# Performance work log

Measured on AMD Instinct MI355X. Metric: run time of the kernel, lower is better.

The kernel has to match this reference:

```python
import jax, jax.numpy as jnp
import numpy as np

BATCH, IN_F, OUT_F, K = 16384, 1024, 1024, 256


def setup_inputs() -> dict:
    key = jax.random.key(0)
    kx, kw, kp = jax.random.split(key, 3)
    x = jax.random.normal(kx, (BATCH, IN_F), dtype=jnp.float32)
    weights = jax.random.normal(kw, (OUT_F, IN_F), dtype=jnp.float32)
    P = jax.random.normal(kp, (K, IN_F), dtype=jnp.float32)  # LSH projection matrix (K, in_features)
    return {"x": x, "weights": weights, "P": P}


def _codes(unit, P):
    # SimHash binary codes in {-1, +1}: sign of random projections
    return jnp.where(unit @ P.T >= 0, 1.0, -1.0).astype(unit.dtype)


def reference(x, weights, P):
    eps = jnp.finfo(x.dtype).eps
    # normalize rows of x and weights
    x_norms = jnp.linalg.norm(x, axis=-1, keepdims=True) + eps        # (B, 1)
    x_unit = x / x_norms
    w_norms = jnp.linalg.norm(weights, axis=-1, keepdims=True) + eps  # (M, 1)
    w_unit = weights / w_norms
    # hash codes
    codes_x = _codes(x_unit, P)   # (B, K)
    codes_w = _codes(w_unit, P)   # (M, K)
    # agreement-based cosine estimate: dot/K = 1 - 2*hamming_frac
    dot = codes_x @ codes_w.T                                   # (B, M)
    k = jnp.asarray(P.shape[0], dtype=x.dtype)
    half_pi = jnp.asarray(np.pi * 0.5, dtype=x.dtype)
    cos_est = jnp.cos(half_pi * (1.0 - dot / k))                # (B, M)
    return x_norms * w_norms.T * cos_est                        # (B, M)
```

## Files before the change

kernel.cpp:

```cpp
#include <hip/hip_runtime.h>
#include <hip/hip_bf16.h>
#include <math.h>

#define BATCH 16384
#define OUTF  1024
#define INF   1024
#define KPROJ 256
#define MTOT  (BATCH + OUTF)

#define GBM 32
#define GBN 128
#define GBK 64
#define NKT (INF / GBK)

#define NZ_THRESH 0.15f

typedef unsigned int       u32;
typedef unsigned long long u64;
typedef unsigned short     u16;
typedef _Float16           f16;
typedef __attribute__((ext_vector_type(8))) _Float16 f16x8;
typedef __attribute__((ext_vector_type(4))) float    f32x4;

#define SCHED0() __builtin_amdgcn_sched_barrier(0)

__device__ __forceinline__ void gl_lds16(const void* g, void* l) {
    __builtin_amdgcn_global_load_lds(
        (const __attribute__((address_space(1))) u32*)g,
        (__attribute__((address_space(3))) u32*)l, 16, 0, 0);
}

__global__ __launch_bounds__(256) void prep_p(const float* __restrict__ P,
                                              f16* __restrict__ Bp) {
    const int wave = threadIdx.x >> 6, lane = threadIdx.x & 63;
    const int pr = blockIdx.x * 4 + wave;
    const float4* v = (const float4*)(P + (size_t)pr * INF);
    ushort4* d = (ushort4*)(Bp + (size_t)pr * INF);
#pragma unroll
    for (int q = 0; q < 4; ++q) {
        float4 f = v[lane + 64 * q];
        ushort4 o;
        o.x = __builtin_bit_cast(u16, (f16)f.x);
        o.y = __builtin_bit_cast(u16, (f16)f.y);
        o.z = __builtin_bit_cast(u16, (f16)f.z);
        o.w = __builtin_bit_cast(u16, (f16)f.w);
        d[lane + 64 * q] = o;
    }
}

__global__ __launch_bounds__(256, 4) void gemm_signs(const float* __restrict__ X,
                                                     const float* __restrict__ W,
                                                     const f16* __restrict__ Bp,
                                                     const float* __restrict__ Pf,
                                                     u64* __restrict__ cx,
                                                     u64* __restrict__ cw,
                                                     float* __restrict__ xn,
                                                     float* __restrict__ wn) {
    __shared__ __align__(16) unsigned char ldsA[GBM * 8 * 16];
    __shared__ __align__(16) unsigned char ldsB[GBN * 8 * 16];
    __shared__ u16 sw[GBM][8];
    __shared__ float nsq[GBM][8];

    const int t    = threadIdx.x;
    const int wid  = t >> 6, lane = t & 63;
    const int l4   = lane >> 4, l15 = lane & 15;
    const int wc   = wid;
    const int sb   = (blockIdx.x & 7) * ((MTOT / GBM) * 2 / 8) + (blockIdx.x >> 3);
    const int bm   = sb >> 1;
    const int bn0  = (sb & 1) * GBN;
    const int am0  = bm * GBM;

    const int ra = t >> 3, sa = t & 7, ca = sa ^ (ra & 7);
    const float* Asrc = (am0 < BATCH) ? X + (size_t)am0 * INF
                                      : W + (size_t)(am0 - BATCH) * INF;
    const float* aRow = Asrc + (size_t)ra * INF + ca * 8;

    const f16* bsrc[4];
#pragma unroll
    for (int i = 0; i < 4; ++i) {
        const int g = (i * 4 + wid) * 64 + lane;
        const int row = g >> 3, sl = g & 7, cb = sl ^ (row & 7);
        bsrc[i] = Bp + (size_t)(bn0 + row) * INF + cb * 8;
    }

    f32x4 acc[2][2] = {};
    float ssq = 0.0f;
    float4 pf0 = *(const float4*)(aRow);
    float4 pf1 = *(const float4*)(aRow + 4);

    for (int kt = 0; kt < NKT; ++kt) {
        ssq += pf0.x * pf0.x + pf0.y * pf0.y + pf0.z * pf0.z + pf0.w * pf0.w +
               pf1.x * pf1.x + pf1.y * pf1.y + pf1.z * pf1.z + pf1.w * pf1.w;
        {
            f16x8 h;
            h[0] = (f16)pf0.x; h[1] = (f16)pf0.y; h[2] = (f16)pf0.z; h[3] = (f16)pf0.w;
            h[4] = (f16)pf1.x; h[5] = (f16)pf1.y; h[6] = (f16)pf1.z; h[7] = (f16)pf1.w;
            *(f16x8*)(ldsA + t * 16) = h;
        }
#pragma unroll
        for (int i = 0; i < 4; ++i)
            gl_lds16(bsrc[i] + kt * GBK, ldsB + (i * 4 + wid) * 1024);
        SCHED0();
        if (kt + 1 < NKT) {
            pf0 = *(const float4*)(aRow + (kt + 1) * GBK);
            pf1 = *(const float4*)(aRow + (kt + 1) * GBK + 4);
            SCHED0();
            asm volatile("s_waitcnt vmcnt(2) lgkmcnt(0)" ::: "memory");
        } else {
            asm volatile("s_waitcnt vmcnt(0) lgkmcnt(0)" ::: "memory");
        }
        SCHED0();
        __builtin_amdgcn_s_barrier();
        SCHED0();
#pragma unroll
        for (int ks = 0; ks < 2; ++ks) {
            f16x8 af[2], bf[2];
#pragma unroll
            for (int i = 0; i < 2; ++i) {
                const int row = i * 16 + l15;
                const int slot = (ks * 4 + l4) ^ (row & 7);
                af[i] = *(const f16x8*)(ldsA + row * 128 + slot * 16);
            }
#pragma unroll
            for (int j = 0; j < 2; ++j) {
                const int col = wc * 32 + j * 16 + l15;
                const int slot = (ks * 4 + l4) ^ (col & 7);
                bf[j] = *(const f16x8*)(ldsB + col * 128 + slot * 16);
            }
#pragma unroll
            for (int i = 0; i < 2; ++i)
#pragma unroll
                for (int j = 0; j < 2; ++j)
                    acc[i][j] = __builtin_amdgcn_mfma_f32_16x16x32_f16(af[i], bf[j], acc[i][j], 0, 0, 0);
        }
        SCHED0();
        __builtin_amdgcn_s_barrier();
        SCHED0();
    }

    nsq[ra][sa] = ssq;

#pragma unroll
    for (int i = 0; i < 2; ++i)
#pragma unroll
        for (int j = 0; j < 2; ++j)
#pragma unroll
            for (int q = 0; q < 4; ++q) {
                const float v = acc[i][j][q];
                int bit = (v >= 0.0f) ? 1 : 0;
                u64 fl = __ballot(fabsf(v) < NZ_THRESH);
                while (fl) {
                    const int src = __ffsll((long long)fl) - 1;
                    fl &= fl - 1;
                    const int lrow = i * 16 + ((src >> 4) << 2) + q;
                    const int col  = bn0 + wc * 32 + j * 16 + (src & 15);
                    const float* xr = Asrc + (size_t)lrow * INF + lane * 16;
                    const float* pr = Pf + (size_t)col * INF + lane * 16;
                    double s = 0.0;
#pragma unroll
                    for (int c4 = 0; c4 < 4; ++c4) {
                        float4 xa = *(const float4*)(xr + c4 * 4);
                        float4 pa = *(const float4*)(pr + c4 * 4);
                        s += (double)xa.x * pa.x + (double)xa.y * pa.y +
                             (double)xa.z * pa.z + (double)xa.w * pa.w;
                    }
#pragma unroll
                    for (int off = 32; off; off >>= 1) s += __shfl_xor(s, off, 64);
                    if (lane == src) bit = (s >= 0.0) ? 1 : 0;
                }
                const u64 b = __ballot(bit != 0);
                if (l15 == 0)
                    sw[i * 16 + l4 * 4 + q][wc * 2 + j] = (u16)(b >> (l4 * 16));
            }
    if (bn0 == 0 && t < GBM) {
        const float* p = nsq[t];
        float s = ((p[0] + p[1]) + (p[2] + p[3])) + ((p[4] + p[5]) + (p[6] + p[7]));
        const float n = sqrtf(s) + 1.1920929e-07f;
        const int grow = am0 + t;
        if (grow < BATCH) xn[grow] = n; else wn[grow - BATCH] = n;
    }
    __syncthreads();
    if (t < 64) {
        const int r = t >> 1, wsel = t & 1;
        const u64 val = *(const u64*)&sw[r][wsel * 4];
        const int grow = am0 + r;
        const int word = (sb & 1) * 2 + wsel;
        if (grow < BATCH) cx[(size_t)grow * 4 + word] = val;
        else              cw[(size_t)(grow - BATCH) * 4 + word] = val;
    }
}

__global__ __launch_bounds__(256) void popc_out(const u64* __restrict__ cx,
                                                const u64* __restrict__ cw,
                                                const float* __restrict__ xn,
                                                const float* __restrict__ wn,
                                                float* __restrict__ out) {
    __shared__ float lut[257];
    __shared__ u64 cxs[64][4];
    __shared__ float xns[64];
    const int t = threadIdx.x;

    lut[t] = (float)cos((double)t * (3.14159265358979323846 / 256.0));
    if (t == 0) lut[256] = -1.0f;

    const int r0 = blockIdx.x * 64;
    cxs[t >> 2][t & 3] = cx[(size_t)r0 * 4 + t];
    if (t < 64) xns[t] = xn[r0 + t];

    const ulonglong4* cwv4 = (const ulonglong4*)cw;
    ulonglong4 c0 = cwv4[4 * t + 0];
    ulonglong4 c1 = cwv4[4 * t + 1];
    ulonglong4 c2 = cwv4[4 * t + 2];
    ulonglong4 c3 = cwv4[4 * t + 3];
    float4 wnr = ((const float4*)wn)[t];

    __syncthreads();

    float4* outv = (float4*)out;
    const size_t obase = (size_t)r0 * (OUTF / 4) + t;
#pragma unroll 4
    for (int r = 0; r < 64; ++r) {
        const u64 a0 = cxs[r][0], a1 = cxs[r][1], a2 = cxs[r][2], a3 = cxs[r][3];
        const float sx = xns[r];
        float4 o;
        o.x = sx * wnr.x * lut[__popcll(a0 ^ c0.x) + __popcll(a1 ^ c0.y) +
                               __popcll(a2 ^ c0.z) + __popcll(a3 ^ c0.w)];
        o.y = sx * wnr.y * lut[__popcll(a0 ^ c1.x) + __popcll(a1 ^ c1.y) +
                               __popcll(a2 ^ c1.z) + __popcll(a3 ^ c1.w)];
        o.z = sx * wnr.z * lut[__popcll(a0 ^ c2.x) + __popcll(a1 ^ c2.y) +
                               __popcll(a2 ^ c2.z) + __popcll(a3 ^ c2.w)];
        o.w = sx * wnr.w * lut[__popcll(a0 ^ c3.x) + __popcll(a1 ^ c3.y) +
                               __popcll(a2 ^ c3.z) + __popcll(a3 ^ c3.w)];
        outv[obase + (size_t)r * (OUTF / 4)] = o;
    }
}

extern "C" void kernel_launch(void* const* d_in, const int* in_sizes, int n_in,
                              void* d_out, int out_size, void* d_ws, size_t ws_size,
                              hipStream_t stream) {
    const float* x = (const float*)d_in[0];
    const float* w = (const float*)d_in[1];
    const float* P = (const float*)d_in[2];
    float* out = (float*)d_out;

    char* ws = (char*)d_ws;
    f16*  Bp = (f16*)ws;
    u64*  cx = (u64*)(ws + 524288);
    u64*  cw = (u64*)(ws + 1048576);
    float* xn = (float*)(ws + 1081344);
    float* wn = (float*)(ws + 1146880);

    prep_p<<<KPROJ / 4, 256, 0, stream>>>(P, Bp);

    gemm_signs<<<(MTOT / GBM) * 2, 256, 0, stream>>>(x, w, Bp, P, cx, cw, xn, wn);

    popc_out<<<BATCH / 64, 256, 0, stream>>>(cx, cw, xn, wn, out);
}
```

Baseline: 61.85 us.

## Double-buffer B tiles and batch A prefetch four k-steps ahead in sign GEMM

Reworks the sign-GEMM main loop into a fully unrolled schedule. The B tile in LDS is now double-buffered, so the next slice's global-to-LDS copy is issued before the current slice's MFMAs run. A-operand fp32 loads are fetched in groups of four k-steps into two alternating register sets. The aim is to hide global load latency behind compute. The cost is more registers and LDS, so the occupancy hint drops from 4 to 3 waves per SIMD, and many steps still wait on vmcnt(0), which may limit the overlap.

```diff
diff --git a/kernel.cpp b/kernel.cpp
--- a/kernel.cpp
+++ b/kernel.cpp
@@ -12,6 +12,7 @@
 #define GBN 128
 #define GBK 64
 #define NKT (INF / GBK)
+#define NWG ((MTOT / GBM) * 2)
 
 #define NZ_THRESH 0.15f
 
@@ -48,7 +49,7 @@
     }
 }
 
-__global__ __launch_bounds__(256, 4) void gemm_signs(const float* __restrict__ X,
+__global__ __launch_bounds__(256, 3) void gemm_signs(const float* __restrict__ X,
                                                      const float* __restrict__ W,
                                                      const f16* __restrict__ Bp,
                                                      const float* __restrict__ Pf,
@@ -57,7 +58,7 @@
                                                      float* __restrict__ xn,
                                                      float* __restrict__ wn) {
     __shared__ __align__(16) unsigned char ldsA[GBM * 8 * 16];
-    __shared__ __align__(16) unsigned char ldsB[GBN * 8 * 16];
+    __shared__ __align__(16) unsigned char ldsB[2 * GBN * 8 * 16];
     __shared__ u16 sw[GBM][8];
     __shared__ float nsq[GBM][8];
 
@@ -65,7 +66,7 @@
     const int wid  = t >> 6, lane = t & 63;
     const int l4   = lane >> 4, l15 = lane & 15;
     const int wc   = wid;
-    const int sb   = (blockIdx.x & 7) * ((MTOT / GBM) * 2 / 8) + (blockIdx.x >> 3);
+    const int sb   = (blockIdx.x & 7) * (NWG / 8) + (blockIdx.x >> 3);
     const int bm   = sb >> 1;
     const int bn0  = (sb & 1) * GBN;
     const int am0  = bm * GBM;
@@ -85,58 +86,107 @@
 
     f32x4 acc[2][2] = {};
     float ssq = 0.0f;
-    float4 pf0 = *(const float4*)(aRow);
-    float4 pf1 = *(const float4*)(aRow + 4);
-
-    for (int kt = 0; kt < NKT; ++kt) {
-        ssq += pf0.x * pf0.x + pf0.y * pf0.y + pf0.z * pf0.z + pf0.w * pf0.w +
-               pf1.x * pf1.x + pf1.y * pf1.y + pf1.z * pf1.z + pf1.w * pf1.w;
-        {
-            f16x8 h;
-            h[0] = (f16)pf0.x; h[1] = (f16)pf0.y; h[2] = (f16)pf0.z; h[3] = (f16)pf0.w;
-            h[4] = (f16)pf1.x; h[5] = (f16)pf1.y; h[6] = (f16)pf1.z; h[7] = (f16)pf1.w;
-            *(f16x8*)(ldsA + t * 16) = h;
-        }
-#pragma unroll
-        for (int i = 0; i < 4; ++i)
-            gl_lds16(bsrc[i] + kt * GBK, ldsB + (i * 4 + wid) * 1024);
-        SCHED0();
-        if (kt + 1 < NKT) {
-            pf0 = *(const float4*)(aRow + (kt + 1) * GBK);
-            pf1 = *(const float4*)(aRow + (kt + 1) * GBK + 4);
-            SCHED0();
-            asm volatile("s_waitcnt vmcnt(2) lgkmcnt(0)" ::: "memory");
-        } else {
-            asm volatile("s_waitcnt vmcnt(0) lgkmcnt(0)" ::: "memory");
-        }
-        SCHED0();
-        __builtin_amdgcn_s_barrier();
-        SCHED0();
-#pragma unroll
-        for (int ks = 0; ks < 2; ++ks) {
-            f16x8 af[2], bf[2];
-#pragma unroll
-            for (int i = 0; i < 2; ++i) {
-                const int row = i * 16 + l15;
-                const int slot = (ks * 4 + l4) ^ (row & 7);
-                af[i] = *(const f16x8*)(ldsA + row * 128 + slot * 16);
-            }
-#pragma unroll
-            for (int j = 0; j < 2; ++j) {
-                const int col = wc * 32 + j * 16 + l15;
-                const int slot = (ks * 4 + l4) ^ (col & 7);
-                bf[j] = *(const f16x8*)(ldsB + col * 128 + slot * 16);
-            }
-#pragma unroll
-            for (int i = 0; i < 2; ++i)
-#pragma unroll
-                for (int j = 0; j < 2; ++j)
-                    acc[i][j] = __builtin_amdgcn_mfma_f32_16x16x32_f16(af[i], bf[j], acc[i][j], 0, 0, 0);
-        }
-        SCHED0();
-        __builtin_amdgcn_s_barrier();
-        SCHED0();
-    }
+    float4 qa0, qa1, qa2, qa3, qa4, qa5, qa6, qa7;
+    float4 qb0, qb1, qb2, qb3, qb4, qb5, qb6, qb7;
+
+#define ALOAD_G(P, G)                                                         \
+    P##0 = *(const float4*)(aRow + ((G) * 4 + 0) * 64);                       \
+    P##1 = *(const float4*)(aRow + ((G) * 4 + 0) * 64 + 4);                   \
+    P##2 = *(const float4*)(aRow + ((G) * 4 + 1) * 64);                       \
+    P##3 = *(const float4*)(aRow + ((G) * 4 + 1) * 64 + 4);                   \
+    P##4 = *(const float4*)(aRow + ((G) * 4 + 2) * 64);                       \
+    P##5 = *(const float4*)(aRow + ((G) * 4 + 2) * 64 + 4);                   \
+    P##6 = *(const float4*)(aRow + ((G) * 4 + 3) * 64);                       \
+    P##7 = *(const float4*)(aRow + ((G) * 4 + 3) * 64 + 4);
+
+#define ASTAGE(Q0, Q1)                                                        \
+    {                                                                         \
+        ssq += Q0.x * Q0.x + Q0.y * Q0.y + Q0.z * Q0.z + Q0.w * Q0.w +        \
+               Q1.x * Q1.x + Q1.y * Q1.y + Q1.z * Q1.z + Q1.w * Q1.w;         \
+        f16x8 h;                                                              \
+        h[0] = (f16)Q0.x; h[1] = (f16)Q0.y; h[2] = (f16)Q0.z; h[3] = (f16)Q0.w;\
+        h[4] = (f16)Q1.x; h[5] = (f16)Q1.y; h[6] = (f16)Q1.z; h[7] = (f16)Q1.w;\
+        *(f16x8*)(ldsA + t * 16) = h;                                         \
+    }
+
+#define BISSUE(S1)                                                            \
+    {                                                                         \
+        _Pragma("unroll")                                                     \
+        for (int i = 0; i < 4; ++i)                                           \
+            gl_lds16(bsrc[i] + (S1) * GBK,                                    \
+                     ldsB + ((S1) & 1) * 16384 + (i * 4 + wid) * 1024);       \
+    }
+
+#define COMPUTE(BOFF)                                                         \
+    {                                                                         \
+        _Pragma("unroll")                                                     \
+        for (int ks = 0; ks < 2; ++ks) {                                      \
+            f16x8 af[2], bf[2];                                               \
+            _Pragma("unroll")                                                 \
+            for (int i = 0; i < 2; ++i) {                                     \
+                const int row = i * 16 + l15;                                 \
+                const int slot = (ks * 4 + l4) ^ (row & 7);                   \
+                af[i] = *(const f16x8*)(ldsA + row * 128 + slot * 16);        \
+            }                                                                 \
+            _Pragma("unroll")                                                 \
+            for (int j = 0; j < 2; ++j) {                                     \
+                const int col = wc * 32 + j * 16 + l15;                       \
+                const int slot = (ks * 4 + l4) ^ (col & 7);                   \
+                bf[j] = *(const f16x8*)(ldsB + (BOFF) + col * 128 + slot * 16);\
+            }                                                                 \
+            _Pragma("unroll")                                                 \
+            for (int i = 0; i < 2; ++i)                                       \
+                _Pragma("unroll")                                             \
+                for (int j = 0; j < 2; ++j)                                   \
+                    acc[i][j] = __builtin_amdgcn_mfma_f32_16x16x32_f16(       \
+                        af[i], bf[j], acc[i][j], 0, 0, 0);                    \
+        }                                                                     \
+    }
+
+#define GSTEP_A(S, Q0, Q1, VM, AP, AG)                                        \
+    ASTAGE(Q0, Q1); SCHED0();                                                 \
+    asm volatile("s_waitcnt vmcnt(" VM ") lgkmcnt(0)" ::: "memory"); SCHED0();\
+    __builtin_amdgcn_s_barrier(); SCHED0();                                   \
+    BISSUE((S) + 1); SCHED0();                                                \
+    ALOAD_G(AP, AG); SCHED0();                                                \
+    COMPUTE(((S) & 1) * 16384); SCHED0();                                     \
+    __builtin_amdgcn_s_barrier(); SCHED0();
+
+#define GSTEP_B(S, Q0, Q1, VM)                                                \
+    ASTAGE(Q0, Q1); SCHED0();                                                 \
+    asm volatile("s_waitcnt vmcnt(" VM ") lgkmcnt(0)" ::: "memory"); SCHED0();\
+    __builtin_amdgcn_s_barrier(); SCHED0();                                   \
+    BISSUE((S) + 1); SCHED0();                                                \
+    COMPUTE(((S) & 1) * 16384); SCHED0();                                     \
+    __builtin_amdgcn_s_barrier(); SCHED0();
+
+#define GSTEP_N(S, Q0, Q1, VM)                                                \
+    ASTAGE(Q0, Q1); SCHED0();                                                 \
+    asm volatile("s_waitcnt vmcnt(" VM ") lgkmcnt(0)" ::: "memory"); SCHED0();\
+    __builtin_amdgcn_s_barrier(); SCHED0();                                   \
+    COMPUTE(((S) & 1) * 16384); SCHED0();                                     \
+    __builtin_amdgcn_s_barrier(); SCHED0();
+
+    BISSUE(0);
+    ALOAD_G(qa, 0);
+    SCHED0();
+
+    GSTEP_A(0,  qa0, qa1, "0", qb, 1);
+    GSTEP_B(1,  qa2, qa3, "8");
+    GSTEP_B(2,  qa4, qa5, "0");
+    GSTEP_B(3,  qa6, qa7, "0");
+    GSTEP_A(4,  qb0, qb1, "0", qa, 2);
+    GSTEP_B(5,  qb2, qb3, "8");
+    GSTEP_B(6,  qb4, qb5, "0");
+    GSTEP_B(7,  qb6, qb7, "0");
+    GSTEP_A(8,  qa0, qa1, "0", qb, 3);
+    GSTEP_B(9,  qa2, qa3, "8");
+    GSTEP_B(10, qa4, qa5, "0");
+    GSTEP_B(11, qa6, qa7, "0");
+    GSTEP_B(12, qb0, qb1, "0");
+    GSTEP_B(13, qb2, qb3, "0");
+    GSTEP_B(14, qb4, qb5, "0");
+    GSTEP_N(15, qb6, qb7, "0");
 
     nsq[ra][sa] = ssq;
 
@@ -252,7 +302,7 @@
 
     prep_p<<<KPROJ / 4, 256, 0, stream>>>(P, Bp);
 
-    gemm_signs<<<(MTOT / GBM) * 2, 256, 0, stream>>>(x, w, Bp, P, cx, cw, xn, wn);
+    gemm_signs<<<NWG, 256, 0, stream>>>(x, w, Bp, P, cx, cw, xn, wn);
 
     popc_out<<<BATCH / 64, 256, 0, stream>>>(cx, cw, xn, wn, out);
 }
```

Result: slower. 67.35 us (+8.9%).
